# Kernel tuning notes

Hardware: AMD Instinct MI355X
Metric: run time of the kernel (lower is better)

The kernel has to match this reference:

```python
import jax, jax.numpy as jnp
import numpy as np

B, L, C, H = 4, 4096, 1024, 16


def setup_inputs() -> dict:
    key = jax.random.key(0)
    k1, k2, k3 = jax.random.split(key, 3)
    x = jax.random.normal(k1, (B, L, C), dtype=jnp.float32)
    # torch nn.Linear params: weight (out, in), bias (out,)
    W_qkv = jax.random.normal(k2, (3 * C, C), dtype=jnp.float32) * 0.02
    b_qkv = jnp.zeros((3 * C,), dtype=jnp.float32)
    W_out = jax.random.normal(k3, (C, C), dtype=jnp.float32) * 0.02
    b_out = jnp.zeros((C,), dtype=jnp.float32)
    return {"x": x, "W_qkv": W_qkv, "b_qkv": b_qkv, "W_out": W_out,
            "b_out": b_out, "num_heads": H}


def reference(x, W_qkv, b_qkv, W_out, b_out, num_heads):
    # Faithful to the source, INCLUDING its head-axis bug:
    # q,k,v stay (B, L, H, D); attention is computed over the HEAD axis
    # (H x H per token), and the final transpose(1,2).reshape scrambles
    # sequence/head layout exactly as torch does.
    b, l, c = x.shape
    h = num_heads
    d = c // h
    scale = d ** (-0.5)
    qkv = (x @ W_qkv.T + b_qkv).reshape(b, l, 3, h, d)
    q, k, v = qkv[:, :, 0], qkv[:, :, 1], qkv[:, :, 2]  # (B, L, H, D)
    # (B,L,H,D) @ (B,L,D,H) -> (B,L,H,H)
    attn = jnp.einsum('blhd,blgd->blhg', q, k) * scale
    attn = jax.nn.softmax(attn, axis=-1)
    # dropout is identity in eval mode
    out = jnp.einsum('blhg,blgd->blhd', attn, v)      # (B, L, H, D)
    out = jnp.swapaxes(out, 1, 2).reshape(b, l, c)    # torch transpose(1,2).reshape
    return out @ W_out.T + b_out
```

## Files before the change

kernel.cpp:

```cpp
#include <hip/hip_runtime.h>
#include <hip/hip_bf16.h>


typedef __attribute__((ext_vector_type(8))) short bf16x8;
typedef __attribute__((ext_vector_type(4))) float f32x4;

__device__ __forceinline__ float bf2f(unsigned short u) {
    union { unsigned int i; float f; } x;
    x.i = ((unsigned int)u) << 16;
    return x.f;
}
__device__ __forceinline__ unsigned short f2bf(float f) {
    unsigned int u = __float_as_uint(f);
    u = (u + 0x7FFFu + ((u >> 16) & 1u)) >> 16;
    return (unsigned short)u;
}

#define VMCNT2() asm volatile("s_waitcnt vmcnt(2)" ::: "memory")
#define VMCNT0() asm volatile("s_waitcnt vmcnt(0)" ::: "memory")
#define BAR()    __builtin_amdgcn_s_barrier()
#define SCHED0() __builtin_amdgcn_sched_barrier(0)

__global__ __launch_bounds__(256) void cast_all(const float* __restrict__ x,
                                                const float* __restrict__ wq,
                                                const float* __restrict__ wo,
                                                unsigned short* __restrict__ xb,
                                                unsigned short* __restrict__ wqb,
                                                unsigned short* __restrict__ wob) {
    const size_t base = (size_t)blockIdx.x * 2048 + threadIdx.x;
#pragma unroll
    for (int it = 0; it < 8; ++it) {
        size_t i = base + (size_t)it * 256;
        const float4* s; ushort4* d; size_t off;
        if (i < 4194304)      { s = (const float4*)x;  d = (ushort4*)xb;  off = i; }
        else if (i < 4980736) { s = (const float4*)wq; d = (ushort4*)wqb; off = i - 4194304; }
        else                  { s = (const float4*)wo; d = (ushort4*)wob; off = i - 4980736; }
        float4 v = s[off];
        ushort4 o;
        o.x = f2bf(v.x); o.y = f2bf(v.y); o.z = f2bf(v.z); o.w = f2bf(v.w);
        d[off] = o;
    }
}

template<int OUTF32>
__global__ __launch_bounds__(1024, 1) void gemm256(const unsigned short* __restrict__ A,
                                                   const unsigned short* __restrict__ B,
                                                   const float* __restrict__ bias,
                                                   unsigned short* __restrict__ Cb,
                                                   float* __restrict__ Cf,
                                                   int M, int N, int K, int NXT) {
    __shared__ __align__(16) unsigned short lds[2][2][2][8192];

    const int tid  = threadIdx.x;
    const int lane = tid & 63;
    const int wave = tid >> 6;
    const int wr = wave >> 2;
    const int wc = wave & 3;
    const int fr = lane & 15;
    const int fq = lane >> 4;
    const int ha = wr >> 1;
    const int hb = wc >> 1;

    const int nwg  = gridDim.x;
    const int orig = blockIdx.x;
    const int wg   = (orig & 7) * (nwg >> 3) + (orig >> 3);
    const int tileM = (wg / NXT) * 256;
    const int tileN = (wg % NXT) * 256;

    const int r8  = tid >> 3;
    const int jsw = (tid & 7) ^ (r8 & 7);
    const unsigned short* Ap = A;
    const unsigned short* Bp = B;

#define STAGE(nb, OPp, HH, ktt) do {                                                   \
    const unsigned short* gb = (OPp) ? Bp : Ap;                                        \
    const int rb = ((OPp) ? tileN : tileM) + (HH) * 128 + r8;                          \
    const unsigned short* s0 = gb + (size_t)rb * K + (ktt) * 64 + jsw * 8;             \
    unsigned short* d0 = &lds[nb][OPp][HH][tid * 8];                                   \
    __builtin_amdgcn_global_load_lds((const __attribute__((address_space(1))) void*)s0,\
        (__attribute__((address_space(3))) void*)d0, 16, 0, 0);                        \
} while (0)

#define READ_K(bb, ks) do {                                                            \
    _Pragma("unroll") for (int i2 = 0; i2 < 4; ++i2) {                                 \
        const int lr = (wr & 1) * 64 + i2 * 16 + fr;                                   \
        af[i2] = *(const bf16x8*)&lds[bb][0][ha][lr * 64 + ((((ks)*4+fq) ^ (lr & 7)) << 3)];\
    }                                                                                  \
    _Pragma("unroll") for (int j2 = 0; j2 < 4; ++j2) {                                 \
        const int lc = (wc & 1) * 64 + j2 * 16 + fr;                                   \
        bf[j2] = *(const bf16x8*)&lds[bb][1][hb][lc * 64 + ((((ks)*4+fq) ^ (lc & 7)) << 3)];\
    }                                                                                  \
} while (0)

#define MFMA_K() do {                                                                  \
    __builtin_amdgcn_s_setprio(1);                                                     \
    _Pragma("unroll") for (int i2 = 0; i2 < 4; ++i2)                                   \
    _Pragma("unroll") for (int j2 = 0; j2 < 4; ++j2)                                   \
        acc[i2][j2] = __builtin_amdgcn_mfma_f32_16x16x32_bf16(af[i2], bf[j2],          \
                                                              acc[i2][j2], 0, 0, 0);   \
    __builtin_amdgcn_s_setprio(0);                                                     \
} while (0)

    f32x4 acc[4][4];
#pragma unroll
    for (int i = 0; i < 4; ++i)
#pragma unroll
        for (int j = 0; j < 4; ++j) acc[i][j] = (f32x4){0.f, 0.f, 0.f, 0.f};

    STAGE(0, 0, 0, 0);
    STAGE(0, 1, 0, 0);
    STAGE(0, 1, 1, 0);
    STAGE(0, 0, 1, 0);

    const int NT = K >> 6;
    int cur = 0;
    for (int kt = 0; kt < NT - 1; ++kt) {
        const int nb = cur ^ 1;
        BAR();
        STAGE(nb, 0, 0, kt + 1);
        STAGE(nb, 1, 0, kt + 1);
        VMCNT2();
        BAR();
        SCHED0();
        bf16x8 af[4], bf[4];
        READ_K(cur, 0); MFMA_K();
        STAGE(nb, 1, 1, kt + 1);
        STAGE(nb, 0, 1, kt + 1);
        READ_K(cur, 1); MFMA_K();
        cur = nb;
    }
    BAR();
    VMCNT0();
    BAR();
    SCHED0();
    {
        bf16x8 af[4], bf[4];
        READ_K(cur, 0); MFMA_K();
        READ_K(cur, 1); MFMA_K();
    }

#pragma unroll
    for (int i = 0; i < 4; ++i) {
        const int row = tileM + wr * 64 + i * 16 + fq * 4;
#pragma unroll
        for (int j = 0; j < 4; ++j) {
            const int col = tileN + wc * 64 + j * 16 + fr;
            const float bv = bias[col];
#pragma unroll
            for (int r = 0; r < 4; ++r) {
                const float v = acc[i][j][r] + bv;
                if (OUTF32) Cf[(size_t)(row + r) * N + col] = v;
                else        Cb[(size_t)(row + r) * N + col] = f2bf(v);
            }
        }
    }
#undef STAGE
#undef READ_K
#undef MFMA_K
}

__global__ __launch_bounds__(256) void attn_kernel(const unsigned short* __restrict__ qkv,
                                                   unsigned short* __restrict__ scr) {
    __shared__ __align__(16) unsigned short sbuf[4][3328];
    __shared__ float Pl[4][256];

    const int wave = threadIdx.x >> 6, lane = threadIdx.x & 63;
    const int token = blockIdx.x * 4 + wave;
    const int b = token >> 12, l = token & 4095;

    const unsigned short* src = qkv + (size_t)token * 3072;
    unsigned short* sw = sbuf[wave];
#pragma unroll
    for (int i = 0; i < 2; ++i) {
        const int c = lane + i * 64;
        const int row = c >> 3, j8 = (c & 7) * 8;
        *(bf16x8*)&sw[row * 72 + j8]        = *(const bf16x8*)&src[c * 8];
        *(bf16x8*)&sw[1152 + row * 72 + j8] = *(const bf16x8*)&src[1024 + c * 8];
        *(bf16x8*)&sw[2304 + c * 8]         = *(const bf16x8*)&src[2048 + c * 8];
    }
    __syncthreads();

    float sv[4];
#pragma unroll
    for (int r = 0; r < 4; ++r) {
        const int p = r * 64 + lane;
        const int h = p >> 4, g = p & 15;
        float acc = 0.f;
#pragma unroll
        for (int d8 = 0; d8 < 8; ++d8) {
            bf16x8 qa = *(const bf16x8*)&sw[h * 72 + d8 * 8];
            bf16x8 kb = *(const bf16x8*)&sw[1152 + g * 72 + d8 * 8];
#pragma unroll
            for (int j = 0; j < 8; ++j)
                acc += bf2f((unsigned short)qa[j]) * bf2f((unsigned short)kb[j]);
        }
        sv[r] = acc * 0.125f;
    }

#pragma unroll
    for (int r = 0; r < 4; ++r) {
        float m = sv[r];
        m = fmaxf(m, __shfl_xor(m, 1));
        m = fmaxf(m, __shfl_xor(m, 2));
        m = fmaxf(m, __shfl_xor(m, 4));
        m = fmaxf(m, __shfl_xor(m, 8));
        float e = __expf(sv[r] - m);
        float s = e;
        s += __shfl_xor(s, 1);
        s += __shfl_xor(s, 2);
        s += __shfl_xor(s, 4);
        s += __shfl_xor(s, 8);
        Pl[wave][r * 64 + lane] = e / s;
    }
    __syncthreads();

    float vreg[16];
#pragma unroll
    for (int g = 0; g < 16; ++g) vreg[g] = bf2f(sw[2304 + g * 64 + lane]);

    const int q_ = l >> 4, j = l & 15;
    const size_t base = ((size_t)b * 4096 + q_) * 1024 + j * 64 + lane;
#pragma unroll
    for (int h = 0; h < 16; ++h) {
        float acc = 0.f;
#pragma unroll
        for (int g = 0; g < 16; ++g) acc += Pl[wave][h * 16 + g] * vreg[g];
        scr[base + (size_t)h * 256 * 1024] = f2bf(acc);
    }
}

extern "C" void kernel_launch(void* const* d_in, const int* in_sizes, int n_in,
                              void* d_out, int out_size, void* d_ws, size_t ws_size,
                              hipStream_t stream) {
    const float* x    = (const float*)d_in[0];
    const float* Wqkv = (const float*)d_in[1];
    const float* bqkv = (const float*)d_in[2];
    const float* Wout = (const float*)d_in[3];
    const float* bout = (const float*)d_in[4];
    float* out = (float*)d_out;

    char* ws = (char*)d_ws;
    unsigned short* xb   = (unsigned short*)(ws);
    unsigned short* wqb  = (unsigned short*)(ws + 33554432);
    unsigned short* wob  = (unsigned short*)(ws + 39845888);
    unsigned short* qkvb = (unsigned short*)(ws + 41943040);
    unsigned short* scr  = (unsigned short*)(ws + 142606336);

    cast_all<<<2560, 256, 0, stream>>>(x, Wqkv, Wout, xb, wqb, wob);

    gemm256<0><<<768, 1024, 0, stream>>>(xb, wqb, bqkv, qkvb, nullptr, 16384, 3072, 1024, 12);

    attn_kernel<<<4096, 256, 0, stream>>>(qkvb, scr);

    gemm256<1><<<256, 1024, 0, stream>>>(scr, wob, bout, nullptr, out, 16384, 1024, 1024, 4);
}
```

Baseline: 198.9 us.

## Use an 8-wave 256x256 GEMM variant for the output projection

Adds a second GEMM kernel that uses 512 threads (8 waves) per 256x256 tile. Each wave computes a 128x64 sub-tile with twice the accumulators and issues two global-to-LDS loads per stage. The output projection now runs on this kernel with launch bounds that allow two workgroups per CU, aiming for better latency hiding and more fragment reuse on the 256-tile grid. The QKV GEMM keeps the 16-wave kernel. In exchange the per-wave register pressure is higher and the pipeline waits on vmcnt(4).

```diff
diff --git a/kernel.cpp b/kernel.cpp
--- a/kernel.cpp
+++ b/kernel.cpp
@@ -16,6 +16,7 @@
     return (unsigned short)u;
 }
 
+#define VMCNT4() asm volatile("s_waitcnt vmcnt(4)" ::: "memory")
 #define VMCNT2() asm volatile("s_waitcnt vmcnt(2)" ::: "memory")
 #define VMCNT0() asm volatile("s_waitcnt vmcnt(0)" ::: "memory")
 #define BAR()    __builtin_amdgcn_s_barrier()
@@ -42,13 +43,11 @@
     }
 }
 
-template<int OUTF32>
-__global__ __launch_bounds__(1024, 1) void gemm256(const unsigned short* __restrict__ A,
-                                                   const unsigned short* __restrict__ B,
-                                                   const float* __restrict__ bias,
-                                                   unsigned short* __restrict__ Cb,
-                                                   float* __restrict__ Cf,
-                                                   int M, int N, int K, int NXT) {
+__global__ __launch_bounds__(1024, 1) void gemm_w16(const unsigned short* __restrict__ A,
+                                                    const unsigned short* __restrict__ B,
+                                                    const float* __restrict__ bias,
+                                                    unsigned short* __restrict__ Cb,
+                                                    int N, int K, int NXT) {
     __shared__ __align__(16) unsigned short lds[2][2][2][8192];
 
     const int tid  = threadIdx.x;
@@ -72,7 +71,7 @@
     const unsigned short* Ap = A;
     const unsigned short* Bp = B;
 
-#define STAGE(nb, OPp, HH, ktt) do {                                                   \
+#define STAGE16(nb, OPp, HH, ktt) do {                                                 \
     const unsigned short* gb = (OPp) ? Bp : Ap;                                        \
     const int rb = ((OPp) ? tileN : tileM) + (HH) * 128 + r8;                          \
     const unsigned short* s0 = gb + (size_t)rb * K + (ktt) * 64 + jsw * 8;             \
@@ -81,7 +80,7 @@
         (__attribute__((address_space(3))) void*)d0, 16, 0, 0);                        \
 } while (0)
 
-#define READ_K(bb, ks) do {                                                            \
+#define READ_K16(bb, ks) do {                                                          \
     _Pragma("unroll") for (int i2 = 0; i2 < 4; ++i2) {                                 \
         const int lr = (wr & 1) * 64 + i2 * 16 + fr;                                   \
         af[i2] = *(const bf16x8*)&lds[bb][0][ha][lr * 64 + ((((ks)*4+fq) ^ (lr & 7)) << 3)];\
@@ -92,7 +91,7 @@
     }                                                                                  \
 } while (0)
 
-#define MFMA_K() do {                                                                  \
+#define MFMA_K16() do {                                                                \
     __builtin_amdgcn_s_setprio(1);                                                     \
     _Pragma("unroll") for (int i2 = 0; i2 < 4; ++i2)                                   \
     _Pragma("unroll") for (int j2 = 0; j2 < 4; ++j2)                                   \
@@ -107,26 +106,26 @@
 #pragma unroll
         for (int j = 0; j < 4; ++j) acc[i][j] = (f32x4){0.f, 0.f, 0.f, 0.f};
 
-    STAGE(0, 0, 0, 0);
-    STAGE(0, 1, 0, 0);
-    STAGE(0, 1, 1, 0);
-    STAGE(0, 0, 1, 0);
+    STAGE16(0, 0, 0, 0);
+    STAGE16(0, 1, 0, 0);
+    STAGE16(0, 1, 1, 0);
+    STAGE16(0, 0, 1, 0);
 
     const int NT = K >> 6;
     int cur = 0;
     for (int kt = 0; kt < NT - 1; ++kt) {
         const int nb = cur ^ 1;
         BAR();
-        STAGE(nb, 0, 0, kt + 1);
-        STAGE(nb, 1, 0, kt + 1);
+        STAGE16(nb, 0, 0, kt + 1);
+        STAGE16(nb, 1, 0, kt + 1);
         VMCNT2();
         BAR();
         SCHED0();
         bf16x8 af[4], bf[4];
-        READ_K(cur, 0); MFMA_K();
-        STAGE(nb, 1, 1, kt + 1);
-        STAGE(nb, 0, 1, kt + 1);
-        READ_K(cur, 1); MFMA_K();
+        READ_K16(cur, 0); MFMA_K16();
+        STAGE16(nb, 1, 1, kt + 1);
+        STAGE16(nb, 0, 1, kt + 1);
+        READ_K16(cur, 1); MFMA_K16();
         cur = nb;
     }
     BAR();
@@ -135,8 +134,8 @@
     SCHED0();
     {
         bf16x8 af[4], bf[4];
-        READ_K(cur, 0); MFMA_K();
-        READ_K(cur, 1); MFMA_K();
+        READ_K16(cur, 0); MFMA_K16();
+        READ_K16(cur, 1); MFMA_K16();
     }
 
 #pragma unroll
@@ -147,16 +146,144 @@
             const int col = tileN + wc * 64 + j * 16 + fr;
             const float bv = bias[col];
 #pragma unroll
-            for (int r = 0; r < 4; ++r) {
-                const float v = acc[i][j][r] + bv;
-                if (OUTF32) Cf[(size_t)(row + r) * N + col] = v;
-                else        Cb[(size_t)(row + r) * N + col] = f2bf(v);
-            }
+            for (int r = 0; r < 4; ++r)
+                Cb[(size_t)(row + r) * N + col] = f2bf(acc[i][j][r] + bv);
         }
     }
-#undef STAGE
-#undef READ_K
-#undef MFMA_K
+#undef STAGE16
+#undef READ_K16
+#undef MFMA_K16
+}
+
+__global__ __launch_bounds__(512, 2) void gemm_w8(const unsigned short* __restrict__ A,
+                                                  const unsigned short* __restrict__ B,
+                                                  const float* __restrict__ bias,
+                                                  float* __restrict__ Cf,
+                                                  int N, int K, int NXT) {
+    __shared__ __align__(16) unsigned short lds[2][2][2][8192];
+
+    const int tid  = threadIdx.x;
+    const int lane = tid & 63;
+    const int wave = tid >> 6;
+    const int wr = wave >> 2;
+    const int wc = wave & 3;
+    const int fr = lane & 15;
+    const int fq = lane >> 4;
+    const int frx = fr & 7;
+
+    const int nwg  = gridDim.x;
+    const int orig = blockIdx.x;
+    const int wg   = (orig & 7) * (nwg >> 3) + (orig >> 3);
+    const int tileM = (wg / NXT) * 256;
+    const int tileN = (wg % NXT) * 256;
+
+    const int r8  = tid >> 3;
+    const int jsw = (tid & 7) ^ (r8 & 7);
+    const unsigned short* Ap = A;
+    const unsigned short* Bp = B;
+
+#define STAGE8(nb, OPp, HH, ktt) do {                                                  \
+    const unsigned short* gb = (OPp) ? Bp : Ap;                                        \
+    const int rb = ((OPp) ? tileN : tileM) + (HH) * 128 + r8;                          \
+    const unsigned short* s0 = gb + (size_t)rb * K + (ktt) * 64 + jsw * 8;             \
+    unsigned short* d0 = &lds[nb][OPp][HH][tid * 8];                                   \
+    __builtin_amdgcn_global_load_lds((const __attribute__((address_space(1))) void*)s0,\
+        (__attribute__((address_space(3))) void*)d0, 16, 0, 0);                        \
+    __builtin_amdgcn_global_load_lds(                                                  \
+        (const __attribute__((address_space(1))) void*)(s0 + (size_t)64 * K),          \
+        (__attribute__((address_space(3))) void*)(d0 + 4096), 16, 0, 0);               \
+} while (0)
+
+#define READ_A8(bb, h) do {                                                            \
+    _Pragma("unroll") for (int i2 = 0; i2 < 4; ++i2) {                                 \
+        const int ar = (wr * 64 + i2 * 16 + fr) * 64;                                  \
+        af[i2][0] = *(const bf16x8*)&lds[bb][0][h][ar + ((fq ^ frx) << 3)];            \
+        af[i2][1] = *(const bf16x8*)&lds[bb][0][h][ar + (((4 + fq) ^ frx) << 3)];      \
+    }                                                                                  \
+} while (0)
+
+#define READ_B8(bb, g) do {                                                            \
+    _Pragma("unroll") for (int j2 = 0; j2 < 2; ++j2) {                                 \
+        const int br = (wc * 32 + j2 * 16 + fr) * 64;                                  \
+        bfr[2*(g)+j2][0] = *(const bf16x8*)&lds[bb][1][g][br + ((fq ^ frx) << 3)];     \
+        bfr[2*(g)+j2][1] = *(const bf16x8*)&lds[bb][1][g][br + (((4 + fq) ^ frx) << 3)];\
+    }                                                                                  \
+} while (0)
+
+#define MFMA_Q8(h, g) do {                                                             \
+    __builtin_amdgcn_s_setprio(1);                                                     \
+    _Pragma("unroll") for (int i2 = 0; i2 < 4; ++i2)                                   \
+    _Pragma("unroll") for (int j2 = 0; j2 < 2; ++j2) {                                 \
+        acc[(h)*4+i2][(g)*2+j2] = __builtin_amdgcn_mfma_f32_16x16x32_bf16(             \
+            af[i2][0], bfr[2*(g)+j2][0], acc[(h)*4+i2][(g)*2+j2], 0, 0, 0);            \
+        acc[(h)*4+i2][(g)*2+j2] = __builtin_amdgcn_mfma_f32_16x16x32_bf16(             \
+            af[i2][1], bfr[2*(g)+j2][1], acc[(h)*4+i2][(g)*2+j2], 0, 0, 0);            \
+    }                                                                                  \
+    __builtin_amdgcn_s_setprio(0);                                                     \
+} while (0)
+
+    f32x4 acc[8][4];
+#pragma unroll
+    for (int i = 0; i < 8; ++i)
+#pragma unroll
+        for (int j = 0; j < 4; ++j) acc[i][j] = (f32x4){0.f, 0.f, 0.f, 0.f};
+
+    STAGE8(0, 0, 0, 0);
+    STAGE8(0, 1, 0, 0);
+    STAGE8(0, 1, 1, 0);
+    STAGE8(0, 0, 1, 0);
+
+    const int NT = K >> 6;
+    int cur = 0;
+    for (int kt = 0; kt < NT - 1; ++kt) {
+        const int nb = cur ^ 1;
+        BAR();
+        STAGE8(nb, 0, 0, kt + 1);
+        STAGE8(nb, 1, 0, kt + 1);
+        VMCNT4();
+        BAR();
+        SCHED0();
+        bf16x8 af[4][2], bfr[4][2];
+        READ_A8(cur, 0); READ_B8(cur, 0); READ_B8(cur, 1);
+        MFMA_Q8(0, 0);
+        STAGE8(nb, 1, 1, kt + 1);
+        STAGE8(nb, 0, 1, kt + 1);
+        MFMA_Q8(0, 1);
+        READ_A8(cur, 1);
+        MFMA_Q8(1, 0);
+        MFMA_Q8(1, 1);
+        cur = nb;
+    }
+    BAR();
+    VMCNT0();
+    BAR();
+    SCHED0();
+    {
+        bf16x8 af[4][2], bfr[4][2];
+        READ_A8(cur, 0); READ_B8(cur, 0); READ_B8(cur, 1);
+        MFMA_Q8(0, 0);
+        MFMA_Q8(0, 1);
+        READ_A8(cur, 1);
+        MFMA_Q8(1, 0);
+        MFMA_Q8(1, 1);
+    }
+
+#pragma unroll
+    for (int i = 0; i < 8; ++i) {
+        const int row = tileM + (i >> 2) * 128 + wr * 64 + (i & 3) * 16 + fq * 4;
+#pragma unroll
+        for (int j = 0; j < 4; ++j) {
+            const int col = tileN + (j >> 1) * 128 + wc * 32 + (j & 1) * 16 + fr;
+            const float bv = bias[col];
+#pragma unroll
+            for (int r = 0; r < 4; ++r)
+                Cf[(size_t)(row + r) * N + col] = acc[i][j][r] + bv;
+        }
+    }
+#undef STAGE8
+#undef READ_A8
+#undef READ_B8
+#undef MFMA_Q8
 }
 
 __global__ __launch_bounds__(256) void attn_kernel(const unsigned short* __restrict__ qkv,
@@ -248,9 +375,9 @@
 
     cast_all<<<2560, 256, 0, stream>>>(x, Wqkv, Wout, xb, wqb, wob);
 
-    gemm256<0><<<768, 1024, 0, stream>>>(xb, wqb, bqkv, qkvb, nullptr, 16384, 3072, 1024, 12);
+    gemm_w16<<<768, 1024, 0, stream>>>(xb, wqb, bqkv, qkvb, 3072, 1024, 12);
 
     attn_kernel<<<4096, 256, 0, stream>>>(qkvb, scr);
 
-    gemm256<1><<<256, 1024, 0, stream>>>(scr, wob, bout, nullptr, out, 16384, 1024, 1024, 4);
-}
+    gemm_w8<<<256, 512, 0, stream>>>(scr, wob, bout, out, 1024, 1024, 4);
+}
```

Result: no change. 199.1 us (+0.1%).
